# Kernel tuning notes

Measured on AMD Instinct MI355X. Metric: run time of the kernel, lower is better.

The kernel has to match this reference:

```python
import jax, jax.numpy as jnp
import numpy as np

B, S, D = 16, 2048, 128  # batch*heads, seq_len, head_dim


def setup_inputs() -> dict:
    key = jax.random.key(0)
    kq, kk, kv, ks = jax.random.split(key, 4)
    q = jax.random.normal(kq, (B, S, D), dtype=jnp.float32)
    k = jax.random.normal(kk, (B, S, D), dtype=jnp.float32)
    v = jax.random.normal(kv, (B, S, D), dtype=jnp.float32)
    # full-shape scale tensor; keep values away from zero (~sqrt(D))
    inv_scale_factor = jax.random.uniform(ks, (B, S, S), dtype=jnp.float32,
                                          minval=8.0, maxval=16.0)
    return {"q": q, "k": k, "v": v,
            "inv_scale_factor": inv_scale_factor,
            "dropout_p": 0}


def reference(q, k, v, inv_scale_factor, dropout_p):
    # qk = q @ k^T  -> [B, Sq, Skv]
    qk = jnp.einsum('bqd,bkd->bqk', q, k)
    # elementwise divide by full-shape tensor (blocks fused SDPA dispatch)
    scaled_qk = qk / inv_scale_factor
    attn = jax.nn.softmax(scaled_qk, axis=-1)
    # dropout with p=0 is the identity (F.dropout scales by 1/(1-p) == 1)
    y = jnp.einsum('bqk,bkd->bqd', attn, v)
    return y
```

## Files before the change

kernel.cpp:

```cpp
#include <hip/hip_runtime.h>
#include <hip/hip_bf16.h>

#define BATCH 16
#define SEQ   2048
#define HD    128
#define QBLK  64
#define KVBLK 32
#define NT    (SEQ / KVBLK)
#define NW    4

typedef __attribute__((ext_vector_type(8))) short bf16x8;
typedef __attribute__((ext_vector_type(4))) float f32x4;
typedef __attribute__((ext_vector_type(4))) short s16x4;

__device__ __forceinline__ short f2bf(float x) {
    __hip_bfloat16 h = __float2bfloat16(x);
    return *reinterpret_cast<short*>(&h);
}

__global__ __launch_bounds__(256, 2)
void attn_fused(const float* __restrict__ Q, const float* __restrict__ K,
                const float* __restrict__ V, const float* __restrict__ ISF,
                float* __restrict__ O)
{
    const int tid  = threadIdx.x;
    const int lane = tid & 63;
    const int wv   = tid >> 6;
    const int lg   = lane >> 4;
    const int lc   = lane & 15;

    const int bidx = blockIdx.x;
    const int b    = bidx >> 5;
    const int q0   = (bidx & 31) * QBLK;

    __shared__ short Klds[2][32 * 128];
    __shared__ short Vtlds[2][128 * 40];
    __shared__ short Plds[NW * 16 * 40];

    bf16x8 qf[4];
    {
        const float* qrow = Q + ((size_t)b * SEQ + q0 + wv * 16 + lc) * HD;
        #pragma unroll
        for (int ks = 0; ks < 4; ++ks) {
            const float* p = qrow + ks * 32 + lg * 8;
            float4 x0 = *reinterpret_cast<const float4*>(p);
            float4 x1 = *reinterpret_cast<const float4*>(p + 4);
            bf16x8 f;
            f[0]=f2bf(x0.x); f[1]=f2bf(x0.y); f[2]=f2bf(x0.z); f[3]=f2bf(x0.w);
            f[4]=f2bf(x1.x); f[5]=f2bf(x1.y); f[6]=f2bf(x1.z); f[7]=f2bf(x1.w);
            qf[ks] = f;
        }
    }

    f32x4 oacc[8];
    #pragma unroll
    for (int i = 0; i < 8; ++i) oacc[i] = (f32x4){0.f, 0.f, 0.f, 0.f};
    float l_part[4] = {0.f, 0.f, 0.f, 0.f};

    const float* kbase = K + (size_t)b * SEQ * HD;
    const float* vbase = V + (size_t)b * SEQ * HD;
    const float* ibase = ISF + ((size_t)b * SEQ + q0 + wv * 16) * SEQ;

    float4 kreg[4];
    float  vreg[4][4];
    float  isf_cur[8], isf_nxt[8];

    auto LOAD = [&](int kv0) {
        const float* kb = kbase + (size_t)kv0 * HD;
        const float* vb = vbase + (size_t)kv0 * HD;
        #pragma unroll
        for (int r = 0; r < 4; ++r) {
            int idx = r * 256 + tid;
            kreg[r] = *reinterpret_cast<const float4*>(kb + (size_t)(idx >> 5) * HD + (idx & 31) * 4);
        }
        #pragma unroll
        for (int r = 0; r < 4; ++r) {
            int idx = r * 256 + tid;
            int d = idx & 127, kq = idx >> 7;
            #pragma unroll
            for (int j = 0; j < 4; ++j)
                vreg[r][j] = vb[(size_t)(kq * 4 + j) * HD + d];
        }
    };
    auto LOAD_ISF = [&](int kv0, float* dst) {
        #pragma unroll
        for (int nt = 0; nt < 2; ++nt)
            #pragma unroll
            for (int r = 0; r < 4; ++r)
                dst[nt * 4 + r] = ibase[(size_t)(lg * 4 + r) * SEQ + kv0 + nt * 16 + lc];
    };
    auto STORE = [&](int buf) {
        #pragma unroll
        for (int r = 0; r < 4; ++r) {
            int idx = r * 256 + tid;
            int kvr = idx >> 5, d4 = idx & 31;
            s16x4 s;
            s[0]=f2bf(kreg[r].x); s[1]=f2bf(kreg[r].y); s[2]=f2bf(kreg[r].z); s[3]=f2bf(kreg[r].w);
            int chunk = (d4 >> 1) ^ (kvr & 7);
            *reinterpret_cast<s16x4*>(&Klds[buf][kvr * 128 + chunk * 8 + (d4 & 1) * 4]) = s;
        }
        #pragma unroll
        for (int r = 0; r < 4; ++r) {
            int idx = r * 256 + tid;
            int d = idx & 127, kq = idx >> 7;
            s16x4 s;
            #pragma unroll
            for (int j = 0; j < 4; ++j) s[j] = f2bf(vreg[r][j]);
            *reinterpret_cast<s16x4*>(&Vtlds[buf][d * 40 + kq * 4]) = s;
        }
    };

    LOAD(0);
    LOAD_ISF(0, isf_cur);
    STORE(0);
    __syncthreads();

    int cur = 0;
    for (int t = 0; t < NT; ++t) {
        const int kv0n = (t + 1) * KVBLK;
        const bool more = (t + 1 < NT);
        if (more) { LOAD(kv0n); LOAD_ISF(kv0n, isf_nxt); }

        f32x4 sacc[2];
        sacc[0] = (f32x4){0.f,0.f,0.f,0.f};
        sacc[1] = (f32x4){0.f,0.f,0.f,0.f};
        #pragma unroll
        for (int nt = 0; nt < 2; ++nt) {
            int n = lc + nt * 16;
            #pragma unroll
            for (int ks = 0; ks < 4; ++ks) {
                int chunk = (ks * 4 + lg) ^ (n & 7);
                bf16x8 bf = *reinterpret_cast<const bf16x8*>(&Klds[cur][n * 128 + chunk * 8]);
                sacc[nt] = __builtin_amdgcn_mfma_f32_16x16x32_bf16(qf[ks], bf, sacc[nt], 0, 0, 0);
            }
        }

        short pb[2][4];
        #pragma unroll
        for (int nt = 0; nt < 2; ++nt)
            #pragma unroll
            for (int r = 0; r < 4; ++r) {
                float sc = sacc[nt][r] * __builtin_amdgcn_rcpf(isf_cur[nt * 4 + r]);
                float p  = __builtin_amdgcn_exp2f(sc * 1.44269504f);
                l_part[r] += p;
                pb[nt][r] = f2bf(p);
            }

        short* pw = &Plds[wv * 16 * 40];
        #pragma unroll
        for (int nt = 0; nt < 2; ++nt)
            #pragma unroll
            for (int r = 0; r < 4; ++r)
                pw[(lg * 4 + r) * 40 + nt * 16 + lc] = pb[nt][r];
        bf16x8 pa = *reinterpret_cast<const bf16x8*>(&pw[lc * 40 + lg * 8]);

        #pragma unroll
        for (int dt = 0; dt < 8; ++dt) {
            bf16x8 vf = *reinterpret_cast<const bf16x8*>(&Vtlds[cur][(lc + dt * 16) * 40 + lg * 8]);
            oacc[dt] = __builtin_amdgcn_mfma_f32_16x16x32_bf16(pa, vf, oacc[dt], 0, 0, 0);
        }

        if (more) STORE(cur ^ 1);
        __syncthreads();
        cur ^= 1;
        #pragma unroll
        for (int i = 0; i < 8; ++i) isf_cur[i] = isf_nxt[i];
    }

    #pragma unroll
    for (int msk = 1; msk < 16; msk <<= 1)
        #pragma unroll
        for (int r = 0; r < 4; ++r)
            l_part[r] += __shfl_xor(l_part[r], msk, 64);

    float* ob = O + ((size_t)b * SEQ + q0 + wv * 16) * HD;
    #pragma unroll
    for (int r = 0; r < 4; ++r) {
        float inv_l = 1.0f / l_part[r];
        float* orow = ob + (size_t)(lg * 4 + r) * HD;
        #pragma unroll
        for (int dt = 0; dt < 8; ++dt)
            orow[lc + dt * 16] = oacc[dt][r] * inv_l;
    }
}

extern "C" void kernel_launch(void* const* d_in, const int* in_sizes, int n_in,
                              void* d_out, int out_size, void* d_ws, size_t ws_size,
                              hipStream_t stream) {
    const float* q   = (const float*)d_in[0];
    const float* k   = (const float*)d_in[1];
    const float* v   = (const float*)d_in[2];
    const float* isf = (const float*)d_in[3];
    float* out = (float*)d_out;
    dim3 grid(BATCH * (SEQ / QBLK));
    attn_fused<<<grid, 256, 0, stream>>>(q, k, v, isf, out);
}
```

Measured before the change: 127.7 us.

## Deepen register prefetch to two tiles ahead with ping-pong register sets

Prefetches K/V/ISF two KV tiles ahead into two alternating register sets, unrolling the loop by two so each global load has a full extra iteration to land before its data is converted and stored to LDS. Replaces __syncthreads with an lgkmcnt-only wait plus s_barrier, precomputes reciprocal times log2e for the scale, and raises wave priority around MFMA sections. This targets memory latency exposure in the streaming loop, at the cost of more live registers, which may hurt occupancy under the 2-blocks-per-CU launch bound or cause spills.

```diff
diff --git a/kernel.cpp b/kernel.cpp
--- a/kernel.cpp
+++ b/kernel.cpp
@@ -16,6 +16,11 @@
 __device__ __forceinline__ short f2bf(float x) {
     __hip_bfloat16 h = __float2bfloat16(x);
     return *reinterpret_cast<short*>(&h);
+}
+
+__device__ __forceinline__ void bar_lgkm() {
+    asm volatile("s_waitcnt lgkmcnt(0)" ::: "memory");
+    __builtin_amdgcn_s_barrier();
 }
 
 __global__ __launch_bounds__(256, 2)
@@ -61,110 +66,134 @@
     const float* vbase = V + (size_t)b * SEQ * HD;
     const float* ibase = ISF + ((size_t)b * SEQ + q0 + wv * 16) * SEQ;
 
-    float4 kreg[4];
-    float  vreg[4][4];
-    float  isf_cur[8], isf_nxt[8];
-
-    auto LOAD = [&](int kv0) {
-        const float* kb = kbase + (size_t)kv0 * HD;
-        const float* vb = vbase + (size_t)kv0 * HD;
-        #pragma unroll
-        for (int r = 0; r < 4; ++r) {
-            int idx = r * 256 + tid;
-            kreg[r] = *reinterpret_cast<const float4*>(kb + (size_t)(idx >> 5) * HD + (idx & 31) * 4);
-        }
-        #pragma unroll
-        for (int r = 0; r < 4; ++r) {
-            int idx = r * 256 + tid;
-            int d = idx & 127, kq = idx >> 7;
-            #pragma unroll
-            for (int j = 0; j < 4; ++j)
-                vreg[r][j] = vb[(size_t)(kq * 4 + j) * HD + d];
-        }
-    };
-    auto LOAD_ISF = [&](int kv0, float* dst) {
-        #pragma unroll
-        for (int nt = 0; nt < 2; ++nt)
-            #pragma unroll
-            for (int r = 0; r < 4; ++r)
-                dst[nt * 4 + r] = ibase[(size_t)(lg * 4 + r) * SEQ + kv0 + nt * 16 + lc];
-    };
-    auto STORE = [&](int buf) {
-        #pragma unroll
-        for (int r = 0; r < 4; ++r) {
-            int idx = r * 256 + tid;
-            int kvr = idx >> 5, d4 = idx & 31;
-            s16x4 s;
-            s[0]=f2bf(kreg[r].x); s[1]=f2bf(kreg[r].y); s[2]=f2bf(kreg[r].z); s[3]=f2bf(kreg[r].w);
-            int chunk = (d4 >> 1) ^ (kvr & 7);
-            *reinterpret_cast<s16x4*>(&Klds[buf][kvr * 128 + chunk * 8 + (d4 & 1) * 4]) = s;
-        }
-        #pragma unroll
-        for (int r = 0; r < 4; ++r) {
-            int idx = r * 256 + tid;
-            int d = idx & 127, kq = idx >> 7;
-            s16x4 s;
-            #pragma unroll
-            for (int j = 0; j < 4; ++j) s[j] = f2bf(vreg[r][j]);
-            *reinterpret_cast<s16x4*>(&Vtlds[buf][d * 40 + kq * 4]) = s;
-        }
-    };
-
-    LOAD(0);
-    LOAD_ISF(0, isf_cur);
-    STORE(0);
-    __syncthreads();
-
-    int cur = 0;
-    for (int t = 0; t < NT; ++t) {
-        const int kv0n = (t + 1) * KVBLK;
-        const bool more = (t + 1 < NT);
-        if (more) { LOAD(kv0n); LOAD_ISF(kv0n, isf_nxt); }
-
-        f32x4 sacc[2];
-        sacc[0] = (f32x4){0.f,0.f,0.f,0.f};
-        sacc[1] = (f32x4){0.f,0.f,0.f,0.f};
-        #pragma unroll
-        for (int nt = 0; nt < 2; ++nt) {
-            int n = lc + nt * 16;
-            #pragma unroll
-            for (int ks = 0; ks < 4; ++ks) {
-                int chunk = (ks * 4 + lg) ^ (n & 7);
-                bf16x8 bf = *reinterpret_cast<const bf16x8*>(&Klds[cur][n * 128 + chunk * 8]);
-                sacc[nt] = __builtin_amdgcn_mfma_f32_16x16x32_bf16(qf[ks], bf, sacc[nt], 0, 0, 0);
-            }
-        }
-
-        short pb[2][4];
-        #pragma unroll
-        for (int nt = 0; nt < 2; ++nt)
-            #pragma unroll
-            for (int r = 0; r < 4; ++r) {
-                float sc = sacc[nt][r] * __builtin_amdgcn_rcpf(isf_cur[nt * 4 + r]);
-                float p  = __builtin_amdgcn_exp2f(sc * 1.44269504f);
-                l_part[r] += p;
-                pb[nt][r] = f2bf(p);
-            }
-
-        short* pw = &Plds[wv * 16 * 40];
-        #pragma unroll
-        for (int nt = 0; nt < 2; ++nt)
-            #pragma unroll
-            for (int r = 0; r < 4; ++r)
-                pw[(lg * 4 + r) * 40 + nt * 16 + lc] = pb[nt][r];
-        bf16x8 pa = *reinterpret_cast<const bf16x8*>(&pw[lc * 40 + lg * 8]);
-
-        #pragma unroll
-        for (int dt = 0; dt < 8; ++dt) {
-            bf16x8 vf = *reinterpret_cast<const bf16x8*>(&Vtlds[cur][(lc + dt * 16) * 40 + lg * 8]);
-            oacc[dt] = __builtin_amdgcn_mfma_f32_16x16x32_bf16(pa, vf, oacc[dt], 0, 0, 0);
-        }
-
-        if (more) STORE(cur ^ 1);
-        __syncthreads();
-        cur ^= 1;
-        #pragma unroll
-        for (int i = 0; i < 8; ++i) isf_cur[i] = isf_nxt[i];
+    float4 kregA[4], kregB[4];
+    float  vregA[4][4], vregB[4][4];
+    float  isfA[8], isfB[8];
+    float  isf_cur[8];
+
+    #define LOADSET(SET, kv0)                                                        \
+        {                                                                            \
+            const float* kb_ = kbase + (size_t)(kv0) * HD;                           \
+            const float* vb_ = vbase + (size_t)(kv0) * HD;                           \
+            _Pragma("unroll")                                                        \
+            for (int r = 0; r < 4; ++r) {                                            \
+                int idx = r * 256 + tid;                                             \
+                kreg##SET[r] = *reinterpret_cast<const float4*>(                     \
+                    kb_ + (size_t)(idx >> 5) * HD + (idx & 31) * 4);                 \
+            }                                                                        \
+            _Pragma("unroll")                                                        \
+            for (int r = 0; r < 4; ++r) {                                            \
+                int idx = r * 256 + tid;                                             \
+                int d_ = idx & 127, kq_ = idx >> 7;                                  \
+                _Pragma("unroll")                                                    \
+                for (int j = 0; j < 4; ++j)                                          \
+                    vreg##SET[r][j] = vb_[(size_t)(kq_ * 4 + j) * HD + d_];          \
+            }                                                                        \
+            _Pragma("unroll")                                                        \
+            for (int nt = 0; nt < 2; ++nt)                                           \
+                _Pragma("unroll")                                                    \
+                for (int r = 0; r < 4; ++r)                                          \
+                    isf##SET[nt * 4 + r] =                                           \
+                        ibase[(size_t)(lg * 4 + r) * SEQ + (kv0) + nt * 16 + lc];    \
+        }
+
+    #define STORESET(SET, buf)                                                       \
+        {                                                                            \
+            _Pragma("unroll")                                                        \
+            for (int r = 0; r < 4; ++r) {                                            \
+                int idx = r * 256 + tid;                                             \
+                int kvr = idx >> 5, d4 = idx & 31;                                   \
+                s16x4 s_;                                                            \
+                s_[0]=f2bf(kreg##SET[r].x); s_[1]=f2bf(kreg##SET[r].y);              \
+                s_[2]=f2bf(kreg##SET[r].z); s_[3]=f2bf(kreg##SET[r].w);              \
+                int chunk = (d4 >> 1) ^ (kvr & 7);                                   \
+                *reinterpret_cast<s16x4*>(                                           \
+                    &Klds[buf][kvr * 128 + chunk * 8 + (d4 & 1) * 4]) = s_;          \
+            }                                                                        \
+            _Pragma("unroll")                                                        \
+            for (int r = 0; r < 4; ++r) {                                            \
+                int idx = r * 256 + tid;                                             \
+                int d_ = idx & 127, kq_ = idx >> 7;                                  \
+                s16x4 s_;                                                            \
+                _Pragma("unroll")                                                    \
+                for (int j = 0; j < 4; ++j) s_[j] = f2bf(vreg##SET[r][j]);           \
+                *reinterpret_cast<s16x4*>(&Vtlds[buf][d_ * 40 + kq_ * 4]) = s_;      \
+            }                                                                        \
+        }
+
+    #define SETISF(SET)                                                              \
+        _Pragma("unroll")                                                            \
+        for (int i = 0; i < 8; ++i)                                                  \
+            isf_cur[i] = __builtin_amdgcn_rcpf(isf##SET[i]) * 1.44269504f;
+
+    #define COMPUTE(buf)                                                             \
+        {                                                                            \
+            f32x4 sacc[2];                                                           \
+            sacc[0] = (f32x4){0.f,0.f,0.f,0.f};                                      \
+            sacc[1] = (f32x4){0.f,0.f,0.f,0.f};                                      \
+            __builtin_amdgcn_s_setprio(1);                                           \
+            _Pragma("unroll")                                                        \
+            for (int nt = 0; nt < 2; ++nt) {                                         \
+                int n_ = lc + nt * 16;                                               \
+                _Pragma("unroll")                                                    \
+                for (int ks = 0; ks < 4; ++ks) {                                     \
+                    int chunk = (ks * 4 + lg) ^ (n_ & 7);                            \
+                    bf16x8 bf_ = *reinterpret_cast<const bf16x8*>(                   \
+                        &Klds[buf][n_ * 128 + chunk * 8]);                           \
+                    sacc[nt] = __builtin_amdgcn_mfma_f32_16x16x32_bf16(              \
+                        qf[ks], bf_, sacc[nt], 0, 0, 0);                             \
+                }                                                                    \
+            }                                                                        \
+            __builtin_amdgcn_s_setprio(0);                                           \
+            short pb[2][4];                                                          \
+            _Pragma("unroll")                                                        \
+            for (int nt = 0; nt < 2; ++nt)                                           \
+                _Pragma("unroll")                                                    \
+                for (int r = 0; r < 4; ++r) {                                        \
+                    float p_ = __builtin_amdgcn_exp2f(                               \
+                        sacc[nt][r] * isf_cur[nt * 4 + r]);                          \
+                    l_part[r] += p_;                                                 \
+                    pb[nt][r] = f2bf(p_);                                            \
+                }                                                                    \
+            short* pw = &Plds[wv * 16 * 40];                                         \
+            _Pragma("unroll")                                                        \
+            for (int nt = 0; nt < 2; ++nt)                                           \
+                _Pragma("unroll")                                                    \
+                for (int r = 0; r < 4; ++r)                                          \
+                    pw[(lg * 4 + r) * 40 + nt * 16 + lc] = pb[nt][r];                \
+            bf16x8 pa = *reinterpret_cast<const bf16x8*>(&pw[lc * 40 + lg * 8]);     \
+            __builtin_amdgcn_s_setprio(1);                                           \
+            _Pragma("unroll")                                                        \
+            for (int dt = 0; dt < 8; ++dt) {                                         \
+                bf16x8 vf = *reinterpret_cast<const bf16x8*>(                        \
+                    &Vtlds[buf][(lc + dt * 16) * 40 + lg * 8]);                      \
+                oacc[dt] = __builtin_amdgcn_mfma_f32_16x16x32_bf16(                  \
+                    pa, vf, oacc[dt], 0, 0, 0);                                      \
+            }                                                                        \
+            __builtin_amdgcn_s_setprio(0);                                           \
+        }
+
+    LOADSET(A, 0);
+    STORESET(A, 0);
+    LOADSET(B, KVBLK);
+    bar_lgkm();
+    SETISF(A);
+
+    for (int t = 0; t < NT; t += 2) {
+        const bool haveA2 = (t + 2 < NT);
+        const bool haveB3 = (t + 3 < NT);
+
+        if (haveA2) LOADSET(A, (t + 2) * KVBLK);
+        COMPUTE(0);
+        STORESET(B, 1);
+        bar_lgkm();
+        SETISF(B);
+
+        if (haveB3) LOADSET(B, (t + 3) * KVBLK);
+        COMPUTE(1);
+        if (haveA2) STORESET(A, 0);
+        bar_lgkm();
+        if (haveA2) SETISF(A);
     }
 
     #pragma unroll
```

Result: faster. 115.8 us (-9.3%).
